# Performance work log

Measured on AMD Instinct MI355X. Metric: run time of the kernel, lower is better.

The kernel has to match this reference:

```python
import jax, jax.numpy as jnp
import numpy as np
import math

HEADS = 16
HIDDEN = 2048
D_K = HIDDEN // HEADS
BATCH = 2
SEQ = 2048
ROPE_THETA = 10000.0


def make_freqs_cis(seq_len, d_k, theta=ROPE_THETA):
    # Llama rotary frequencies; returned as (seq, d_k//2, 2) = (cos, sin)
    inv_freq = 1.0 / (theta ** (np.arange(0, d_k, 2, dtype=np.float32) / d_k))
    t = np.arange(seq_len, dtype=np.float32)
    ang = np.outer(t, inv_freq)  # (seq, d_k//2)
    return jnp.asarray(np.stack([np.cos(ang), np.sin(ang)], axis=-1))


def setup_inputs() -> dict:
    key = jax.random.key(0)
    ks = jax.random.split(key, 5)
    scale = 1.0 / math.sqrt(HIDDEN)
    return {
        "x": jax.random.normal(ks[0], (BATCH, SEQ, HIDDEN), dtype=jnp.float32),
        "freqs_cis": make_freqs_cis(SEQ, D_K),
        "wq": jax.random.normal(ks[1], (HIDDEN, HIDDEN), dtype=jnp.float32) * scale,
        "wk": jax.random.normal(ks[2], (HIDDEN, HIDDEN), dtype=jnp.float32) * scale,
        "wv": jax.random.normal(ks[3], (HIDDEN, HIDDEN), dtype=jnp.float32) * scale,
        "wo": jax.random.normal(ks[4], (HIDDEN, HIDDEN), dtype=jnp.float32) * scale,
    }


def _apply_rope(t, cos, sin):
    # t: (B, S, h, d_k); cos/sin: (1, S, 1, d_k//2)
    B, S, h, dk = t.shape
    tp = t.reshape(B, S, h, dk // 2, 2)
    t0, t1 = tp[..., 0], tp[..., 1]
    r0 = t0 * cos - t1 * sin
    r1 = t0 * sin + t1 * cos
    return jnp.stack([r0, r1], axis=-1).reshape(B, S, h, dk)


def reference(x, freqs_cis, wq, wk, wv, wo):
    B, S, H = x.shape
    h, dk = HEADS, H // HEADS
    # nn.Linear(bias=False): y = x @ W.T
    q = (x @ wq.T).reshape(B, S, h, dk)
    k = (x @ wk.T).reshape(B, S, h, dk)
    v = (x @ wv.T).reshape(B, S, h, dk)
    cos = freqs_cis[None, :, None, :, 0]
    sin = freqs_cis[None, :, None, :, 1]
    q = _apply_rope(q, cos, sin)
    k = _apply_rope(k, cos, sin)
    # (B, h, S, dk)
    q = q.transpose(0, 2, 1, 3)
    k = k.transpose(0, 2, 1, 3)
    v = v.transpose(0, 2, 1, 3)
    scores = jnp.einsum("bhqd,bhkd->bhqk", q, k) / math.sqrt(dk)
    causal = jnp.tril(jnp.ones((S, S), dtype=bool))
    scores = jnp.where(causal[None, None], scores, -jnp.inf)
    attn = jax.nn.softmax(scores, axis=-1)
    out = jnp.einsum("bhqk,bhkd->bhqd", attn, v)
    out = out.transpose(0, 2, 1, 3).reshape(B, S, H)
    return out @ wo.T
```

## Files before the change

kernel.cpp:

```cpp
#include <hip/hip_runtime.h>

#define SEQ 2048
#define HID 2048
#define NH 16
#define DK 128
#define NTOK 4096

typedef __bf16 bf16x8 __attribute__((ext_vector_type(8)));
typedef float f32x4 __attribute__((ext_vector_type(4)));
typedef unsigned int u32x4 __attribute__((ext_vector_type(4)));

__device__ __forceinline__ unsigned short f2bf(float f) {
  unsigned int u = __builtin_bit_cast(unsigned int, f);
  u += 0x7fffu + ((u >> 16) & 1u);
  return (unsigned short)(u >> 16);
}
__device__ __forceinline__ float bf2f(unsigned int lo16) {
  return __builtin_bit_cast(float, lo16 << 16);
}

__device__ __forceinline__ void async_cp16(const void* g, void* l) {
  __builtin_amdgcn_global_load_lds(
      (__attribute__((address_space(1))) void*)const_cast<void*>(g),
      (__attribute__((address_space(3))) void*)l, 16, 0, 0);
}

__global__ void convert_all_kernel(const float* __restrict__ x,
                                   const float* __restrict__ wq,
                                   const float* __restrict__ wk,
                                   const float* __restrict__ wv,
                                   const float* __restrict__ wo,
                                   unsigned short* __restrict__ xb,
                                   unsigned short* __restrict__ wqb,
                                   unsigned short* __restrict__ wkb,
                                   unsigned short* __restrict__ wvb,
                                   unsigned short* __restrict__ wob) {
  const int bid = blockIdx.x;
  const float* src;
  unsigned short* dst;
  int base;
  if (bid < 8192) {
    src = x; dst = xb; base = bid;
  } else {
    const int t = (bid - 8192) >> 12;
    base = (bid - 8192) & 4095;
    src = (t == 0) ? wq : (t == 1) ? wk : (t == 2) ? wv : wo;
    dst = (t == 0) ? wqb : (t == 1) ? wkb : (t == 2) ? wvb : wob;
  }
  const int i = base * 256 + threadIdx.x;
  float4 v = ((const float4*)src)[i];
  ushort4 o;
  o.x = f2bf(v.x); o.y = f2bf(v.y); o.z = f2bf(v.z); o.w = f2bf(v.w);
  ((ushort4*)dst)[i] = o;
}

template<bool F32OUT>
__global__ __launch_bounds__(256, 3)
void gemm_bt_kernel(const unsigned short* __restrict__ A,
                    const unsigned short* __restrict__ B0,
                    const unsigned short* __restrict__ B1,
                    const unsigned short* __restrict__ B2,
                    unsigned short* __restrict__ O0,
                    unsigned short* __restrict__ O1,
                    unsigned short* __restrict__ O2,
                    float* __restrict__ Of,
                    const float* __restrict__ fc) {
  __shared__ alignas(16) unsigned short As[128 * 64];
  __shared__ alignas(16) unsigned short Bs[128 * 64];

  const int bx = blockIdx.x, by = blockIdx.y;
  const unsigned short* B;
  unsigned short* Ob = nullptr;
  int sel = 0, col0;
  if (F32OUT) {
    B = B0;
    col0 = bx * 128;
  } else {
    sel = bx >> 4;
    B = (sel == 0) ? B0 : (sel == 1) ? B1 : B2;
    Ob = (sel == 0) ? O0 : (sel == 1) ? O1 : O2;
    col0 = (bx & 15) * 128;
  }
  const int row0 = by * 128;

  const int tid = threadIdx.x;
  const int wave = tid >> 6, lane = tid & 63;
  const int quad = lane >> 4, r = lane & 15;
  const int wm = wave >> 1, wn = wave & 1;
  const int jbase = wave * 256 + lane;

  f32x4 acc[4][4] = {};

  for (int k0 = 0; k0 < HID; k0 += 64) {
    for (int t = 0; t < 4; ++t) {
      const int j = jbase + t * 64;
      const int m = j >> 3;
      const int gc = (j & 7) ^ (m & 7);
      async_cp16(A + (size_t)(row0 + m) * HID + k0 + gc * 8, As + j * 8);
      async_cp16(B + (size_t)(col0 + m) * HID + k0 + gc * 8, Bs + j * 8);
    }
    __syncthreads();
    for (int kk = 0; kk < 2; ++kk) {
      bf16x8 af[4], bfr[4];
      for (int mt = 0; mt < 4; ++mt) {
        const int m = wm * 64 + mt * 16 + r;
        const int slot = (kk * 4 + quad) ^ (m & 7);
        af[mt] = __builtin_bit_cast(bf16x8, *(const u32x4*)(As + m * 64 + slot * 8));
      }
      for (int nt = 0; nt < 4; ++nt) {
        const int n = wn * 64 + nt * 16 + r;
        const int slot = (kk * 4 + quad) ^ (n & 7);
        bfr[nt] = __builtin_bit_cast(bf16x8, *(const u32x4*)(Bs + n * 64 + slot * 8));
      }
      for (int mt = 0; mt < 4; ++mt)
        for (int nt = 0; nt < 4; ++nt)
          acc[mt][nt] = __builtin_amdgcn_mfma_f32_16x16x32_bf16(
              af[mt], bfr[nt], acc[mt][nt], 0, 0, 0);
    }
    __syncthreads();
  }

  if (!F32OUT && sel == 2) {
    for (int mt = 0; mt < 4; ++mt) {
      const int row = row0 + wm * 64 + mt * 16 + quad * 4;
      const int b = row >> 11, s = row & (SEQ - 1);
      for (int nt = 0; nt < 4; ++nt) {
        const int col = col0 + wn * 64 + nt * 16 + r;
        ushort4 pk;
        pk.x = f2bf(acc[mt][nt][0]);
        pk.y = f2bf(acc[mt][nt][1]);
        pk.z = f2bf(acc[mt][nt][2]);
        pk.w = f2bf(acc[mt][nt][3]);
        *(ushort4*)(Ob + ((size_t)(b * HID + col)) * SEQ + s) = pk;
      }
    }
    return;
  }

  if (!F32OUT) {
    const float qs = (sel == 0) ? 0.08838834764831845f : 1.0f;
    for (int mt = 0; mt < 4; ++mt) {
      const int row = row0 + wm * 64 + mt * 16 + quad * 4;
      for (int nt = 0; nt < 4; ++nt) {
        const int col = col0 + wn * 64 + nt * 16 + r;
        const int d = (wn * 64 + nt * 16 + r) >> 1;
        for (int v = 0; v < 4; ++v) {
          const int s = (row + v) & (SEQ - 1);
          const float2 cs = *(const float2*)(fc + s * 128 + 2 * d);
          const float val = acc[mt][nt][v];
          const float par = __shfl_xor(val, 1, 64);
          const float res = (r & 1) ? (par * cs.y + val * cs.x)
                                    : (val * cs.x - par * cs.y);
          Ob[(size_t)(row + v) * HID + col] = f2bf(res * qs);
        }
      }
    }
    return;
  }

  for (int mt = 0; mt < 4; ++mt) {
    const int row = row0 + wm * 64 + mt * 16 + quad * 4;
    for (int nt = 0; nt < 4; ++nt) {
      const int col = col0 + wn * 64 + nt * 16 + r;
      for (int v = 0; v < 4; ++v)
        Of[(size_t)(row + v) * HID + col] = acc[mt][nt][v];
    }
  }
}

__global__ __launch_bounds__(256, 2)
void flash_attn_kernel(const unsigned short* __restrict__ Qb,
                       const unsigned short* __restrict__ Kb,
                       const unsigned short* __restrict__ VtG,
                       unsigned short* __restrict__ Ob) {
  __shared__ alignas(16) unsigned short KsA[64 * 128];
  __shared__ alignas(16) unsigned short KsB[64 * 128];
  __shared__ alignas(16) unsigned short VsA[128 * 64];
  __shared__ alignas(16) unsigned short VsB[128 * 64];
  __shared__ alignas(16) unsigned short Ps[4][16 * 64];

  const int bx = blockIdx.x, bh = blockIdx.y;
  const int tid = threadIdx.x, wave = tid >> 6, lane = tid & 63;
  const int quad = lane >> 4, r = lane & 15;
  const int tokbase = (bh >> 4) * SEQ;
  const int h = bh & 15;

  const u32x4 onesv = {0x3F803F80u, 0x3F803F80u, 0x3F803F80u, 0x3F803F80u};

  auto stage = [&](int kt, unsigned short* Ks, unsigned short* Vs) {
    for (int t = 0; t < 4; ++t) {
      const int j = t * 256 + tid;
      const int n = j >> 4, slot = j & 15;
      const int gc = (slot & 8) | ((slot & 7) ^ (n & 7));
      async_cp16(Kb + (size_t)(tokbase + kt * 64 + n) * HID + h * DK + gc * 8,
                 Ks + j * 8);
    }
    for (int t = 0; t < 4; ++t) {
      const int j = t * 256 + tid;
      const int d = j >> 3, slot = j & 7;
      const int gc = slot ^ (d & 7);
      async_cp16(VtG + ((size_t)(bh * DK + d)) * SEQ + kt * 64 + gc * 8,
                 Vs + j * 8);
    }
  };

  for (int phase = 0; phase < 2; ++phase) {
    const int qt = phase ? (31 - bx) : bx;
    const int q0 = qt * 64;

    u32x4 qf[4];
    {
      const unsigned short* qrow =
          Qb + (size_t)(tokbase + q0 + wave * 16 + r) * HID + h * DK;
      for (int kk = 0; kk < 4; ++kk)
        qf[kk] = *(const u32x4*)(qrow + kk * 32 + quad * 8);
    }

    f32x4 o[8] = {};
    float m_i[4], l_i[4];
    for (int v = 0; v < 4; ++v) { m_i[v] = -__builtin_inff(); l_i[v] = 0.f; }

    auto body = [&](const unsigned short* Ks, const unsigned short* Vs, int kt) {
      f32x4 s[4];
      for (int nt = 0; nt < 4; ++nt) {
        f32x4 a = {};
        const int n = nt * 16 + r;
        for (int kk = 0; kk < 4; ++kk) {
          const int c = kk * 4 + quad;
          const int slot = (c & 8) | ((c & 7) ^ (r & 7));
          u32x4 bkf = *(const u32x4*)(Ks + n * 128 + slot * 8);
          a = __builtin_amdgcn_mfma_f32_16x16x32_bf16(
              __builtin_bit_cast(bf16x8, qf[kk]),
              __builtin_bit_cast(bf16x8, bkf), a, 0, 0, 0);
        }
        s[nt] = a;
      }

      if (kt == qt) {
        const int qrow_g = q0 + wave * 16 + quad * 4;
        for (int nt = 0; nt < 4; ++nt) {
          const int col = kt * 64 + nt * 16 + r;
          for (int v = 0; v < 4; ++v)
            if (col > qrow_g + v) s[nt][v] = -__builtin_inff();
        }
      }

      float mx[4];
      for (int v = 0; v < 4; ++v)
        mx[v] = fmaxf(fmaxf(s[0][v], s[1][v]), fmaxf(s[2][v], s[3][v]));
      for (int off = 1; off < 16; off <<= 1)
        for (int v = 0; v < 4; ++v)
          mx[v] = fmaxf(mx[v], __shfl_xor(mx[v], off, 64));

      float alpha[4];
      for (int v = 0; v < 4; ++v) {
        const float mnew = fmaxf(m_i[v], mx[v]);
        alpha[v] = __expf(m_i[v] - mnew);
        m_i[v] = mnew;
      }

      unsigned short* ps = &Ps[wave][0];
      for (int nt = 0; nt < 4; ++nt) {
        const int chunk = nt * 2 + (r >> 3);
        for (int v = 0; v < 4; ++v) {
          const float p = __expf(s[nt][v] - m_i[v]);
          const int row = quad * 4 + v;
          const int slot = chunk ^ (row & 7);
          ps[row * 64 + slot * 8 + (r & 7)] = f2bf(p);
        }
      }
      for (int dt = 0; dt < 8; ++dt)
        for (int v = 0; v < 4; ++v)
          o[dt][v] *= alpha[v];
      __asm__ volatile("" ::: "memory");

      f32x4 rsacc = {};
      for (int kk2 = 0; kk2 < 2; ++kk2) {
        const int c = kk2 * 4 + quad;
        const int aslot = c ^ (r & 7);
        u32x4 pa = *(const u32x4*)(ps + r * 64 + aslot * 8);
        rsacc = __builtin_amdgcn_mfma_f32_16x16x32_bf16(
            __builtin_bit_cast(bf16x8, pa),
            __builtin_bit_cast(bf16x8, onesv), rsacc, 0, 0, 0);
        for (int dt = 0; dt < 8; ++dt) {
          const int d = dt * 16 + r;
          const int bslot = c ^ (d & 7);
          u32x4 bv = *(const u32x4*)(Vs + d * 64 + bslot * 8);
          o[dt] = __builtin_amdgcn_mfma_f32_16x16x32_bf16(
              __builtin_bit_cast(bf16x8, pa),
              __builtin_bit_cast(bf16x8, bv), o[dt], 0, 0, 0);
        }
      }
      for (int v = 0; v < 4; ++v)
        l_i[v] = l_i[v] * alpha[v] + rsacc[v];
    };

    stage(0, KsA, VsA);
    int kt = 0;
    while (true) {
      __syncthreads();
      if (kt + 1 <= qt) stage(kt + 1, KsB, VsB);
      body(KsA, VsA, kt);
      if (++kt > qt) break;
      __syncthreads();
      if (kt + 1 <= qt) stage(kt + 1, KsA, VsA);
      body(KsB, VsB, kt);
      if (++kt > qt) break;
    }

    float li[4];
    for (int v = 0; v < 4; ++v) li[v] = 1.f / l_i[v];
    for (int dt = 0; dt < 8; ++dt)
      for (int v = 0; v < 4; ++v) {
        const size_t row = (size_t)tokbase + q0 + wave * 16 + quad * 4 + v;
        Ob[row * HID + h * DK + dt * 16 + r] = f2bf(o[dt][v] * li[v]);
      }
    __syncthreads();
  }
}

extern "C" void kernel_launch(void* const* d_in, const int* in_sizes, int n_in,
                              void* d_out, int out_size, void* d_ws, size_t ws_size,
                              hipStream_t stream) {
  const float* x  = (const float*)d_in[0];
  const float* fc = (const float*)d_in[1];
  const float* wq = (const float*)d_in[2];
  const float* wk = (const float*)d_in[3];
  const float* wv = (const float*)d_in[4];
  const float* wo = (const float*)d_in[5];
  float* out = (float*)d_out;

  unsigned short* xb  = (unsigned short*)d_ws;
  unsigned short* wqb = xb  + (size_t)NTOK * HID;
  unsigned short* wkb = wqb + (size_t)HID * HID;
  unsigned short* wvb = wkb + (size_t)HID * HID;
  unsigned short* wob = wvb + (size_t)HID * HID;
  unsigned short* qb  = wob + (size_t)HID * HID;
  unsigned short* kb  = qb  + (size_t)NTOK * HID;
  unsigned short* vtb = kb  + (size_t)NTOK * HID;
  unsigned short* ab  = vtb + (size_t)NTOK * HID;

  convert_all_kernel<<<8192 + 4 * 4096, 256, 0, stream>>>(
      x, wq, wk, wv, wo, xb, wqb, wkb, wvb, wob);

  gemm_bt_kernel<false><<<dim3(48, 32), 256, 0, stream>>>(
      xb, wqb, wkb, wvb, qb, kb, vtb, nullptr, fc);

  flash_attn_kernel<<<dim3(16, 32), 256, 0, stream>>>(qb, kb, vtb, ab);

  gemm_bt_kernel<true><<<dim3(16, 32), 256, 0, stream>>>(
      ab, wob, nullptr, nullptr, nullptr, nullptr, nullptr, out, fc);
}
```

Before: 368.6 us.

## Pack RoPE table to bf16, fold log2e into Q scale, relax GEMM occupancy

The convert kernel now also packs the cos/sin table into one bf16 pair per uint32, so the QKV GEMM epilogue reads half as many bytes per rotation. The Q scale now includes log2(e), which lets the flash-attention softmax use exp2f instead of __expf. The GEMM launch bounds drop from 3 to 2 blocks per SM, giving the compiler more registers per thread. These changes trade some RoPE precision for less memory traffic and fewer softmax instructions, and the lower occupancy target may reduce latency hiding.

```diff
diff --git a/kernel.cpp b/kernel.cpp
--- a/kernel.cpp
+++ b/kernel.cpp
@@ -30,12 +30,21 @@
                                    const float* __restrict__ wk,
                                    const float* __restrict__ wv,
                                    const float* __restrict__ wo,
+                                   const float* __restrict__ fc,
                                    unsigned short* __restrict__ xb,
                                    unsigned short* __restrict__ wqb,
                                    unsigned short* __restrict__ wkb,
                                    unsigned short* __restrict__ wvb,
-                                   unsigned short* __restrict__ wob) {
+                                   unsigned short* __restrict__ wob,
+                                   unsigned int* __restrict__ fcb) {
   const int bid = blockIdx.x;
+  if (bid >= 24576) {
+    const int idx = (bid - 24576) * 256 + threadIdx.x;
+    const int s = idx >> 6, d = idx & 63;
+    const float2 cs = *(const float2*)(fc + s * 128 + 2 * d);
+    fcb[idx] = (unsigned int)f2bf(cs.x) | ((unsigned int)f2bf(cs.y) << 16);
+    return;
+  }
   const float* src;
   unsigned short* dst;
   int base;
@@ -55,7 +64,7 @@
 }
 
 template<bool F32OUT>
-__global__ __launch_bounds__(256, 3)
+__global__ __launch_bounds__(256, 2)
 void gemm_bt_kernel(const unsigned short* __restrict__ A,
                     const unsigned short* __restrict__ B0,
                     const unsigned short* __restrict__ B1,
@@ -64,7 +73,7 @@
                     unsigned short* __restrict__ O1,
                     unsigned short* __restrict__ O2,
                     float* __restrict__ Of,
-                    const float* __restrict__ fc) {
+                    const unsigned int* __restrict__ fcb) {
   __shared__ alignas(16) unsigned short As[128 * 64];
   __shared__ alignas(16) unsigned short Bs[128 * 64];
 
@@ -138,7 +147,7 @@
   }
 
   if (!F32OUT) {
-    const float qs = (sel == 0) ? 0.08838834764831845f : 1.0f;
+    const float qs = (sel == 0) ? 0.12751743f : 1.0f;
     for (int mt = 0; mt < 4; ++mt) {
       const int row = row0 + wm * 64 + mt * 16 + quad * 4;
       for (int nt = 0; nt < 4; ++nt) {
@@ -146,11 +155,12 @@
         const int d = (wn * 64 + nt * 16 + r) >> 1;
         for (int v = 0; v < 4; ++v) {
           const int s = (row + v) & (SEQ - 1);
-          const float2 cs = *(const float2*)(fc + s * 128 + 2 * d);
+          const unsigned int u = fcb[s * 64 + d];
+          const float c = bf2f(u & 0xffffu), sn = bf2f(u >> 16);
           const float val = acc[mt][nt][v];
           const float par = __shfl_xor(val, 1, 64);
-          const float res = (r & 1) ? (par * cs.y + val * cs.x)
-                                    : (val * cs.x - par * cs.y);
+          const float res = (r & 1) ? (par * sn + val * c)
+                                    : (val * c - par * sn);
           Ob[(size_t)(row + v) * HID + col] = f2bf(res * qs);
         }
       }
@@ -255,7 +265,7 @@
       float alpha[4];
       for (int v = 0; v < 4; ++v) {
         const float mnew = fmaxf(m_i[v], mx[v]);
-        alpha[v] = __expf(m_i[v] - mnew);
+        alpha[v] = exp2f(m_i[v] - mnew);
         m_i[v] = mnew;
       }
 
@@ -263,7 +273,7 @@
       for (int nt = 0; nt < 4; ++nt) {
         const int chunk = nt * 2 + (r >> 3);
         for (int v = 0; v < 4; ++v) {
-          const float p = __expf(s[nt][v] - m_i[v]);
+          const float p = exp2f(s[nt][v] - m_i[v]);
           const int row = quad * 4 + v;
           const int slot = chunk ^ (row & 7);
           ps[row * 64 + slot * 8 + (r & 7)] = f2bf(p);
@@ -339,15 +349,16 @@
   unsigned short* kb  = qb  + (size_t)NTOK * HID;
   unsigned short* vtb = kb  + (size_t)NTOK * HID;
   unsigned short* ab  = vtb + (size_t)NTOK * HID;
-
-  convert_all_kernel<<<8192 + 4 * 4096, 256, 0, stream>>>(
-      x, wq, wk, wv, wo, xb, wqb, wkb, wvb, wob);
+  unsigned int*   fcb = (unsigned int*)(ab + (size_t)NTOK * HID);
+
+  convert_all_kernel<<<24576 + 512, 256, 0, stream>>>(
+      x, wq, wk, wv, wo, fc, xb, wqb, wkb, wvb, wob, fcb);
 
   gemm_bt_kernel<false><<<dim3(48, 32), 256, 0, stream>>>(
-      xb, wqb, wkb, wvb, qb, kb, vtb, nullptr, fc);
+      xb, wqb, wkb, wvb, qb, kb, vtb, nullptr, fcb);
 
   flash_attn_kernel<<<dim3(16, 32), 256, 0, stream>>>(qb, kb, vtb, ab);
 
   gemm_bt_kernel<true><<<dim3(16, 32), 256, 0, stream>>>(
-      ab, wob, nullptr, nullptr, nullptr, nullptr, nullptr, out, fc);
-}
+      ab, wob, nullptr, nullptr, nullptr, nullptr, nullptr, out, fcb);
+}
```

Result: faster. 354.9 us (-3.7%).
